# Kernel optimization log

Measured on AMD Instinct MI355X. Metric: run time of the kernel, lower is better.

The kernel has to match this reference:

```python
import jax, jax.numpy as jnp
import numpy as np


def setup_inputs() -> dict:
    key = jax.random.key(0)
    ks = jax.random.split(key, 8)
    B, T, D, S, E, V = 8, 64, 1024, 32, 16, 50257
    SCALE = 0.02  # keep dot-products in a sane range for softmax
    return {
        "decoder_states": jax.random.normal(ks[0], (B, T, D), jnp.float32),
        "scene_memory": jax.random.normal(ks[1], (B, S, D), jnp.float32),
        "embedding_weight": jax.random.normal(ks[2], (V, D), jnp.float32) * SCALE,
        "ent_ids": jax.random.randint(ks[3], (B, S, E), 0, V, jnp.int32),
        "Wq": jax.random.normal(ks[4], (D, D), jnp.float32) * SCALE,
        "bq": jnp.zeros((D,), jnp.float32),
        "Wk": jax.random.normal(ks[5], (D, D), jnp.float32) * SCALE,
        "bk": jnp.zeros((D,), jnp.float32),
        "Wp": jax.random.normal(ks[6], (2 * D, 1), jnp.float32) * SCALE,
        "bp": jnp.full((1,), 3.0, jnp.float32),  # nn.init.constant_(bias, 3.0)
    }


def reference(decoder_states, scene_memory, embedding_weight, ent_ids,
              Wq, bq, Wk, bk, Wp, bp):
    B, T, D = decoder_states.shape
    S = scene_memory.shape[1]
    V = embedding_weight.shape[0]

    # scene-level attention
    q = decoder_states @ Wq + bq            # [B,T,D]
    k = scene_memory @ Wk + bk              # [B,S,D]
    scores = jnp.einsum('btd,bsd->bts', q, k) / jnp.sqrt(jnp.float32(D))
    scene_attn = jax.nn.softmax(scores, axis=-1)          # [B,T,S]
    context = jnp.einsum('bts,bsd->btd', scene_attn, scene_memory)

    # hard p_gen gate
    gate_in = jnp.concatenate([decoder_states, context], axis=-1)  # [B,T,2D]
    p_gen = jax.nn.sigmoid((gate_in @ Wp + bp - 0.5) * 10.0)       # [B,T,1]

    # entity salience per scene, scattered into V-sized tensor
    dec_last = decoder_states[:, -1, :]                   # [B,D]
    ent_embs = embedding_weight[ent_ids]                  # [B,S,E,D] gather
    salience = jax.nn.softmax(
        jnp.einsum('bd,bsed->bse', dec_last, ent_embs), axis=-1)  # [B,S,E]
    bi = jnp.arange(B)[:, None, None]
    si = jnp.arange(S)[None, :, None]
    scene_to_token = jnp.zeros((B, S, V), decoder_states.dtype)
    scene_to_token = scene_to_token.at[bi, si, ent_ids].set(salience)

    pointer_probs = jnp.einsum('bts,bsv->btv', scene_attn, scene_to_token)
    return p_gen, pointer_probs
```

## Files before the change

### kernel.cpp

```cpp
#include <hip/hip_runtime.h>
#include <hip/hip_bf16.h>
#include <math.h>

#define BB 8
#define TT 64
#define DD 1024
#define SS 32
#define EE 16
#define VV 50257
#define BT (BB*TT)
#define BS (BB*SS)

typedef __attribute__((ext_vector_type(8))) short short8;
typedef __attribute__((ext_vector_type(4))) float floatx4;

static __device__ inline unsigned short f2bf(float x) {
    __hip_bfloat16 h = __float2bfloat16(x);
    union { __hip_bfloat16 h; unsigned short u; } cv; cv.h = h;
    return cv.u;
}

static __device__ inline void gl_lds16(const void* g, void* l) {
    __builtin_amdgcn_global_load_lds(
        (const __attribute__((address_space(1))) void*)g,
        (__attribute__((address_space(3))) void*)l, 16, 0, 0);
}

__global__ __launch_bounds__(256) void prep_kernel(
    const float* __restrict__ dec, const float* __restrict__ scene,
    const float* __restrict__ Wq, const float* __restrict__ Wk,
    const float* __restrict__ Wp,
    unsigned short* __restrict__ Xb, unsigned short* __restrict__ Wt,
    float* __restrict__ dw, float* __restrict__ mw)
{
    __shared__ float tile[64][65];
    const int bid = blockIdx.x;
    const int t = threadIdx.x;
    if (bid < 768) {
        const int row = bid;
        const float* src = (row < BT) ? dec + (size_t)row * DD
                                      : scene + (size_t)(row - BT) * DD;
        const float4 v = *(const float4*)&src[t * 4];
        ushort4 u;
        u.x = f2bf(v.x); u.y = f2bf(v.y); u.z = f2bf(v.z); u.w = f2bf(v.w);
        *(ushort4*)&Xb[(size_t)row * DD + t * 4] = u;
    } else if (bid < 1280) {
        const int tb = bid - 768;
        const int sel = tb >> 8;
        const int tt8 = tb & 255;
        const int k0 = (tt8 >> 4) * 64, n0 = (tt8 & 15) * 64;
        const float* Wsrc = sel ? Wk : Wq;
        const int c4 = (t & 15) * 4;
        #pragma unroll
        for (int i = 0; i < 4; ++i) {
            const int r = (t >> 4) + 16 * i;
            const float4 v = *(const float4*)&Wsrc[(size_t)(k0 + r) * DD + n0 + c4];
            tile[r][c4 + 0] = v.x; tile[r][c4 + 1] = v.y;
            tile[r][c4 + 2] = v.z; tile[r][c4 + 3] = v.w;
        }
        __syncthreads();
        #pragma unroll
        for (int i = 0; i < 4; ++i) {
            const int n = (t >> 4) + 16 * i;
            ushort4 u;
            u.x = f2bf(tile[c4 + 0][n]); u.y = f2bf(tile[c4 + 1][n]);
            u.z = f2bf(tile[c4 + 2][n]); u.w = f2bf(tile[c4 + 3][n]);
            *(ushort4*)&Wt[(size_t)sel * DD * DD + (size_t)(n0 + n) * DD + k0 + c4] = u;
        }
    } else {
        const int di = bid - 1280;
        const float* x; const float* wp; float* outp;
        if (di < BT) { x = dec   + (size_t)di * DD;        wp = Wp;      outp = dw + di; }
        else         { x = scene + (size_t)(di - BT) * DD; wp = Wp + DD; outp = mw + (di - BT); }
        float s = 0.f;
        #pragma unroll
        for (int i = 0; i < 4; ++i) s += x[t + 256 * i] * wp[t + 256 * i];
        for (int off = 32; off; off >>= 1) s += __shfl_down(s, off);
        if ((t & 63) == 0) tile[0][t >> 6] = s;
        __syncthreads();
        if (t == 0) *outp = tile[0][0] + tile[0][1] + tile[0][2] + tile[0][3];
    }
}

__global__ __launch_bounds__(128) void gemm_mfma(
    const unsigned short* __restrict__ Xb, const unsigned short* __restrict__ Wt,
    const float* __restrict__ bq, const float* __restrict__ bk,
    float* __restrict__ qo, float* __restrict__ ko)
{
    __shared__ unsigned short As[32 * 32];
    __shared__ unsigned short Bs[64 * 32];
    const int bid = blockIdx.x;
    const int bm = bid >> 4;
    const int bn = bid & 15;
    const int m0 = bm * 32, n0 = bn * 64;
    const bool isq = (bm < 16);
    const unsigned short* Wsel = Wt + (isq ? 0 : (size_t)DD * DD);
    const int tid = threadIdx.x;
    const int w = tid >> 6, l = tid & 63;

    const int arow = 16 * w + (l >> 2);
    const int kb8  = (l & 3) * 8;
    floatx4 acc[4] = {{0.f,0.f,0.f,0.f},{0.f,0.f,0.f,0.f},
                      {0.f,0.f,0.f,0.f},{0.f,0.f,0.f,0.f}};

    for (int k0 = 0; k0 < DD; k0 += 32) {
        __syncthreads();
        gl_lds16(&Xb[(size_t)(m0 + arow) * DD + k0 + kb8], &As[w * 512]);
        #pragma unroll
        for (int i = 0; i < 2; ++i) {
            const int brow = 32 * w + 16 * i + (l >> 2);
            gl_lds16(&Wsel[(size_t)(n0 + brow) * DD + k0 + kb8],
                     &Bs[w * 1024 + i * 512]);
        }
        __syncthreads();
        const short8 a = *(const short8*)&As[(16 * w + (l & 15)) * 32 + (l >> 4) * 8];
        #pragma unroll
        for (int j = 0; j < 4; ++j) {
            const short8 b = *(const short8*)&Bs[(16 * j + (l & 15)) * 32 + (l >> 4) * 8];
            acc[j] = __builtin_amdgcn_mfma_f32_16x16x32_bf16(a, b, acc[j], 0, 0, 0);
        }
    }
    #pragma unroll
    for (int j = 0; j < 4; ++j) {
        const int gcol = n0 + 16 * j + (l & 15);
        const float bias = isq ? bq[gcol] : bk[gcol];
        #pragma unroll
        for (int r = 0; r < 4; ++r) {
            const int grow = m0 + 16 * w + (l >> 4) * 4 + r;
            const float val = acc[j][r] + bias;
            if (isq) qo[(size_t)grow * DD + gcol] = val;
            else     ko[(size_t)(grow - BT) * DD + gcol] = val;
        }
    }
}

__global__ __launch_bounds__(256) void attn_sal_kernel(
    const float* __restrict__ qm, const float* __restrict__ km,
    const float* __restrict__ dec, const float* __restrict__ emb,
    const int* __restrict__ ids,
    const float* __restrict__ dwv, const float* __restrict__ mwv,
    const float* __restrict__ bp,
    float* __restrict__ attn_out, float* __restrict__ pgen_out,
    float* __restrict__ sal_out)
{
    __shared__ __align__(16) float qs[DD];
    __shared__ float sc[SS];
    __shared__ int lid[EE];
    const int tid = threadIdx.x;
    const int w = tid >> 6, lane = tid & 63;

    if (blockIdx.x < BT) {
        const int bt = blockIdx.x;
        const int b  = bt / TT;
        *(float4*)&qs[tid * 4] = *(const float4*)&qm[(size_t)bt * DD + tid * 4];
        __syncthreads();
        for (int j = 0; j < 8; ++j) {
            const int s = w * 8 + j;
            const float* kr = km + (size_t)(b * SS + s) * DD;
            float accv = 0.f;
            #pragma unroll
            for (int i = 0; i < 4; ++i) {
                const float4 qv = *(const float4*)&qs[4 * lane + 256 * i];
                const float4 kv = *(const float4*)&kr[4 * lane + 256 * i];
                accv += qv.x * kv.x + qv.y * kv.y + qv.z * kv.z + qv.w * kv.w;
            }
            for (int off = 32; off; off >>= 1) accv += __shfl_down(accv, off);
            if (lane == 0) sc[s] = accv * 0.03125f;
        }
        __syncthreads();
        if (tid < 64) {
            float v = (lane < SS) ? sc[lane] : -INFINITY;
            float m = v;
            for (int off = 32; off; off >>= 1) m = fmaxf(m, __shfl_xor(m, off));
            float e = (lane < SS) ? __expf(v - m) : 0.f;
            float sum = e;
            for (int off = 32; off; off >>= 1) sum += __shfl_xor(sum, off);
            const float a = e / sum;
            float g = (lane < SS) ? a * mwv[b * SS + lane] : 0.f;
            for (int off = 32; off; off >>= 1) g += __shfl_xor(g, off);
            if (lane < SS) attn_out[bt * SS + lane] = a;
            if (lane == 0) {
                const float z = dwv[bt] + g + bp[0] - 0.5f;
                pgen_out[bt] = 1.0f / (1.0f + __expf(-10.0f * z));
            }
        }
    } else {
        const int bs = blockIdx.x - BT;
        const int b  = bs / SS;
        const float* dl = dec + (size_t)(b * TT + (TT - 1)) * DD;
        *(float4*)&qs[tid * 4] = *(const float4*)&dl[tid * 4];
        if (tid < EE) lid[tid] = ids[bs * EE + tid];
        __syncthreads();
        for (int j = 0; j < 4; ++j) {
            const int e = w * 4 + j;
            const float* er = emb + (size_t)lid[e] * DD;
            float accv = 0.f;
            #pragma unroll
            for (int i = 0; i < 4; ++i) {
                const float4 dv = *(const float4*)&qs[4 * lane + 256 * i];
                const float4 ev = *(const float4*)&er[4 * lane + 256 * i];
                accv += dv.x * ev.x + dv.y * ev.y + dv.z * ev.z + dv.w * ev.w;
            }
            for (int off = 32; off; off >>= 1) accv += __shfl_down(accv, off);
            if (lane == 0) sc[e] = accv;
        }
        __syncthreads();
        if (tid == 0) {
            float m = -INFINITY;
            for (int e = 0; e < EE; ++e) m = fmaxf(m, sc[e]);
            float ex[EE]; float sum = 0.f;
            for (int e = 0; e < EE; ++e) { ex[e] = __expf(sc[e] - m); sum += ex[e]; }
            const float inv = 1.0f / sum;
            for (int e = 0; e < EE; ++e) {
                bool dup = false;
                for (int e2 = e + 1; e2 < EE; ++e2)
                    if (lid[e2] == lid[e]) { dup = true; break; }
                sal_out[bs * EE + e] = dup ? 0.f : ex[e] * inv;
            }
        }
    }
}

__global__ __launch_bounds__(256) void pp_kernel(
    const float* __restrict__ attn, const float* __restrict__ sal,
    const int* __restrict__ ids, float* __restrict__ pp)
{
    __shared__ float at[SS];
    const int bt = blockIdx.x;
    const int b  = bt / TT;
    const int tid = threadIdx.x;
    if (tid < SS) at[tid] = attn[bt * SS + tid];
    float* row = pp + (size_t)bt * VV;
    const int h = (4 - (bt & 3)) & 3;
    if (tid < h) row[tid] = 0.f;
    const int nv = (VV - h) >> 2;
    float4* rv = (float4*)(row + h);
    const float4 z4 = make_float4(0.f, 0.f, 0.f, 0.f);
    for (int i = tid; i < nv; i += 256) rv[i] = z4;
    const int tail = (VV - h) & 3;
    if (tid < tail) row[h + 4 * nv + tid] = 0.f;
    __syncthreads();
    for (int i = tid; i < SS * EE; i += 256) {
        const int s = i >> 4, e = i & 15;
        const float v = at[s] * sal[(b * SS + s) * EE + e];
        atomicAdd(&row[ids[(b * SS + s) * EE + e]], v);
    }
}

extern "C" void kernel_launch(void* const* d_in, const int* in_sizes, int n_in,
                              void* d_out, int out_size, void* d_ws, size_t ws_size,
                              hipStream_t stream) {
    (void)in_sizes; (void)n_in; (void)ws_size; (void)out_size;
    const float* dec   = (const float*)d_in[0];
    const float* scene = (const float*)d_in[1];
    const float* emb   = (const float*)d_in[2];
    const int*   ids   = (const int*)  d_in[3];
    const float* Wq    = (const float*)d_in[4];
    const float* bq    = (const float*)d_in[5];
    const float* Wk    = (const float*)d_in[6];
    const float* bk    = (const float*)d_in[7];
    const float* Wp    = (const float*)d_in[8];
    const float* bp    = (const float*)d_in[9];
    float* out = (float*)d_out;
    float* ws  = (float*)d_ws;

    float* q    = ws;
    float* kbuf = q    + 512 * 1024;
    float* attn = kbuf + 256 * 1024;
    float* sal  = attn + 512 * 32;
    float* dw   = sal  + 256 * 16;
    float* mw   = dw   + 512;
    unsigned short* Xb = (unsigned short*)(mw + 256);
    unsigned short* Wt = Xb + 768 * 1024;

    prep_kernel<<<2048, 256, 0, stream>>>(dec, scene, Wq, Wk, Wp, Xb, Wt, dw, mw);
    gemm_mfma<<<384, 128, 0, stream>>>(Xb, Wt, bq, bk, q, kbuf);
    attn_sal_kernel<<<768, 256, 0, stream>>>(q, kbuf, dec, emb, ids, dw, mw, bp,
                                             attn, out, sal);
    pp_kernel<<<512, 256, 0, stream>>>(attn, sal, ids, out + 512);
}
```

Before: 327.4 us.

## Distribute pointer-prob zeroing across earlier kernels as extra blocks

The roughly 100 MB zero-fill of the pointer_probs output moves out of the final scatter kernel. It is split into three ranges, each handled by extra blocks appended to the prep, GEMM and attention kernels, so the memset overlaps with compute-bound blocks. The scatter kernel then only does the atomic adds. This relies on the float4 view of the output being aligned, since out+512 floats is 16-byte aligned. The extra blocks may compete with the compute blocks for bandwidth and occupancy.

```diff
diff --git a/kernel.cpp b/kernel.cpp
--- a/kernel.cpp
+++ b/kernel.cpp
@@ -11,6 +11,13 @@
 #define BT (BB*TT)
 #define BS (BB*SS)
 
+#define N4TOT 6432896
+#define Z0END 2144300
+#define Z1END 4288600
+#define ZB0 512
+#define ZB1 1024
+#define ZB2 512
+
 typedef __attribute__((ext_vector_type(8))) short short8;
 typedef __attribute__((ext_vector_type(4))) float floatx4;
 
@@ -24,6 +31,13 @@
     __builtin_amdgcn_global_load_lds(
         (const __attribute__((address_space(1))) void*)g,
         (__attribute__((address_space(3))) void*)l, 16, 0, 0);
+}
+
+static __device__ inline void zero_range(float4* pv, int start, int end,
+                                         int zb, int nzb, int nthr) {
+    const float4 z4 = make_float4(0.f, 0.f, 0.f, 0.f);
+    for (int i = start + zb * nthr + (int)threadIdx.x; i < end; i += nzb * nthr)
+        pv[i] = z4;
 }
 
 __global__ __launch_bounds__(256) void prep_kernel(
@@ -31,7 +45,8 @@
     const float* __restrict__ Wq, const float* __restrict__ Wk,
     const float* __restrict__ Wp,
     unsigned short* __restrict__ Xb, unsigned short* __restrict__ Wt,
-    float* __restrict__ dw, float* __restrict__ mw)
+    float* __restrict__ dw, float* __restrict__ mw,
+    float* __restrict__ pp)
 {
     __shared__ float tile[64][65];
     const int bid = blockIdx.x;
@@ -67,7 +82,7 @@
             u.z = f2bf(tile[c4 + 2][n]); u.w = f2bf(tile[c4 + 3][n]);
             *(ushort4*)&Wt[(size_t)sel * DD * DD + (size_t)(n0 + n) * DD + k0 + c4] = u;
         }
-    } else {
+    } else if (bid < 2048) {
         const int di = bid - 1280;
         const float* x; const float* wp; float* outp;
         if (di < BT) { x = dec   + (size_t)di * DD;        wp = Wp;      outp = dw + di; }
@@ -79,17 +94,24 @@
         if ((t & 63) == 0) tile[0][t >> 6] = s;
         __syncthreads();
         if (t == 0) *outp = tile[0][0] + tile[0][1] + tile[0][2] + tile[0][3];
+    } else {
+        zero_range((float4*)pp, 0, Z0END, bid - 2048, ZB0, 256);
     }
 }
 
 __global__ __launch_bounds__(128) void gemm_mfma(
     const unsigned short* __restrict__ Xb, const unsigned short* __restrict__ Wt,
     const float* __restrict__ bq, const float* __restrict__ bk,
-    float* __restrict__ qo, float* __restrict__ ko)
+    float* __restrict__ qo, float* __restrict__ ko,
+    float* __restrict__ pp)
 {
     __shared__ unsigned short As[32 * 32];
     __shared__ unsigned short Bs[64 * 32];
     const int bid = blockIdx.x;
+    if (bid >= 384) {
+        zero_range((float4*)pp, Z0END, Z1END, bid - 384, ZB1, 128);
+        return;
+    }
     const int bm = bid >> 4;
     const int bn = bid & 15;
     const int m0 = bm * 32, n0 = bn * 64;
@@ -141,7 +163,7 @@
     const float* __restrict__ dwv, const float* __restrict__ mwv,
     const float* __restrict__ bp,
     float* __restrict__ attn_out, float* __restrict__ pgen_out,
-    float* __restrict__ sal_out)
+    float* __restrict__ sal_out, float* __restrict__ pp)
 {
     __shared__ __align__(16) float qs[DD];
     __shared__ float sc[SS];
@@ -184,7 +206,7 @@
                 pgen_out[bt] = 1.0f / (1.0f + __expf(-10.0f * z));
             }
         }
-    } else {
+    } else if (blockIdx.x < BT + BS) {
         const int bs = blockIdx.x - BT;
         const int b  = bs / SS;
         const float* dl = dec + (size_t)(b * TT + (TT - 1)) * DD;
@@ -218,10 +240,12 @@
                 sal_out[bs * EE + e] = dup ? 0.f : ex[e] * inv;
             }
         }
-    }
-}
-
-__global__ __launch_bounds__(256) void pp_kernel(
+    } else {
+        zero_range((float4*)pp, Z1END, N4TOT, blockIdx.x - (BT + BS), ZB2, 256);
+    }
+}
+
+__global__ __launch_bounds__(256) void scatter_kernel(
     const float* __restrict__ attn, const float* __restrict__ sal,
     const int* __restrict__ ids, float* __restrict__ pp)
 {
@@ -230,16 +254,8 @@
     const int b  = bt / TT;
     const int tid = threadIdx.x;
     if (tid < SS) at[tid] = attn[bt * SS + tid];
+    __syncthreads();
     float* row = pp + (size_t)bt * VV;
-    const int h = (4 - (bt & 3)) & 3;
-    if (tid < h) row[tid] = 0.f;
-    const int nv = (VV - h) >> 2;
-    float4* rv = (float4*)(row + h);
-    const float4 z4 = make_float4(0.f, 0.f, 0.f, 0.f);
-    for (int i = tid; i < nv; i += 256) rv[i] = z4;
-    const int tail = (VV - h) & 3;
-    if (tid < tail) row[h + 4 * nv + tid] = 0.f;
-    __syncthreads();
     for (int i = tid; i < SS * EE; i += 256) {
         const int s = i >> 4, e = i & 15;
         const float v = at[s] * sal[(b * SS + s) * EE + e];
@@ -263,6 +279,7 @@
     const float* bp    = (const float*)d_in[9];
     float* out = (float*)d_out;
     float* ws  = (float*)d_ws;
+    float* pp  = out + 512;
 
     float* q    = ws;
     float* kbuf = q    + 512 * 1024;
@@ -273,9 +290,10 @@
     unsigned short* Xb = (unsigned short*)(mw + 256);
     unsigned short* Wt = Xb + 768 * 1024;
 
-    prep_kernel<<<2048, 256, 0, stream>>>(dec, scene, Wq, Wk, Wp, Xb, Wt, dw, mw);
-    gemm_mfma<<<384, 128, 0, stream>>>(Xb, Wt, bq, bk, q, kbuf);
-    attn_sal_kernel<<<768, 256, 0, stream>>>(q, kbuf, dec, emb, ids, dw, mw, bp,
-                                             attn, out, sal);
-    pp_kernel<<<512, 256, 0, stream>>>(attn, sal, ids, out + 512);
-}
+    prep_kernel<<<2048 + ZB0, 256, 0, stream>>>(dec, scene, Wq, Wk, Wp,
+                                                Xb, Wt, dw, mw, pp);
+    gemm_mfma<<<384 + ZB1, 128, 0, stream>>>(Xb, Wt, bq, bk, q, kbuf, pp);
+    attn_sal_kernel<<<768 + ZB2, 256, 0, stream>>>(q, kbuf, dec, emb, ids,
+                                                   dw, mw, bp, attn, out, sal, pp);
+    scatter_kernel<<<512, 256, 0, stream>>>(attn, sal, ids, pp);
+}
```

New measurement: 328.2 us. No clear change (+0.3%).

## Fuse attention into pointer scatter, move salience into prep, double-buffer GEMM

Applied to the files above, without the earlier changes.

Salience computation moves from the attention kernel into the prep kernel as extra blocks, since it depends only on the inputs. Scene attention, the softmax and p_gen are fused into the pointer-probability kernel, which removes the attn round trip and one launch. The Q/K GEMM now uses 64x64 tiles with 256 threads and double-buffered LDS staging to prefetch the next K slice while computing. Risks are fewer GEMM blocks (192) lowering occupancy, and longer per-block work in the fused kernel.

```diff
diff --git a/kernel.cpp b/kernel.cpp
--- a/kernel.cpp
+++ b/kernel.cpp
@@ -29,11 +29,13 @@
 __global__ __launch_bounds__(256) void prep_kernel(
     const float* __restrict__ dec, const float* __restrict__ scene,
     const float* __restrict__ Wq, const float* __restrict__ Wk,
-    const float* __restrict__ Wp,
+    const float* __restrict__ Wp, const float* __restrict__ emb,
+    const int* __restrict__ ids,
     unsigned short* __restrict__ Xb, unsigned short* __restrict__ Wt,
-    float* __restrict__ dw, float* __restrict__ mw)
+    float* __restrict__ dw, float* __restrict__ mw,
+    float* __restrict__ sal_out)
 {
-    __shared__ float tile[64][65];
+    __shared__ __align__(16) float tile[64][65];
     const int bid = blockIdx.x;
     const int t = threadIdx.x;
     if (bid < 768) {
@@ -67,7 +69,7 @@
             u.z = f2bf(tile[c4 + 2][n]); u.w = f2bf(tile[c4 + 3][n]);
             *(ushort4*)&Wt[(size_t)sel * DD * DD + (size_t)(n0 + n) * DD + k0 + c4] = u;
         }
-    } else {
+    } else if (bid < 2048) {
         const int di = bid - 1280;
         const float* x; const float* wp; float* outp;
         if (di < BT) { x = dec   + (size_t)di * DD;        wp = Wp;      outp = dw + di; }
@@ -79,137 +81,37 @@
         if ((t & 63) == 0) tile[0][t >> 6] = s;
         __syncthreads();
         if (t == 0) *outp = tile[0][0] + tile[0][1] + tile[0][2] + tile[0][3];
-    }
-}
-
-__global__ __launch_bounds__(128) void gemm_mfma(
-    const unsigned short* __restrict__ Xb, const unsigned short* __restrict__ Wt,
-    const float* __restrict__ bq, const float* __restrict__ bk,
-    float* __restrict__ qo, float* __restrict__ ko)
-{
-    __shared__ unsigned short As[32 * 32];
-    __shared__ unsigned short Bs[64 * 32];
-    const int bid = blockIdx.x;
-    const int bm = bid >> 4;
-    const int bn = bid & 15;
-    const int m0 = bm * 32, n0 = bn * 64;
-    const bool isq = (bm < 16);
-    const unsigned short* Wsel = Wt + (isq ? 0 : (size_t)DD * DD);
-    const int tid = threadIdx.x;
-    const int w = tid >> 6, l = tid & 63;
-
-    const int arow = 16 * w + (l >> 2);
-    const int kb8  = (l & 3) * 8;
-    floatx4 acc[4] = {{0.f,0.f,0.f,0.f},{0.f,0.f,0.f,0.f},
-                      {0.f,0.f,0.f,0.f},{0.f,0.f,0.f,0.f}};
-
-    for (int k0 = 0; k0 < DD; k0 += 32) {
-        __syncthreads();
-        gl_lds16(&Xb[(size_t)(m0 + arow) * DD + k0 + kb8], &As[w * 512]);
-        #pragma unroll
-        for (int i = 0; i < 2; ++i) {
-            const int brow = 32 * w + 16 * i + (l >> 2);
-            gl_lds16(&Wsel[(size_t)(n0 + brow) * DD + k0 + kb8],
-                     &Bs[w * 1024 + i * 512]);
-        }
-        __syncthreads();
-        const short8 a = *(const short8*)&As[(16 * w + (l & 15)) * 32 + (l >> 4) * 8];
-        #pragma unroll
-        for (int j = 0; j < 4; ++j) {
-            const short8 b = *(const short8*)&Bs[(16 * j + (l & 15)) * 32 + (l >> 4) * 8];
-            acc[j] = __builtin_amdgcn_mfma_f32_16x16x32_bf16(a, b, acc[j], 0, 0, 0);
-        }
-    }
-    #pragma unroll
-    for (int j = 0; j < 4; ++j) {
-        const int gcol = n0 + 16 * j + (l & 15);
-        const float bias = isq ? bq[gcol] : bk[gcol];
-        #pragma unroll
-        for (int r = 0; r < 4; ++r) {
-            const int grow = m0 + 16 * w + (l >> 4) * 4 + r;
-            const float val = acc[j][r] + bias;
-            if (isq) qo[(size_t)grow * DD + gcol] = val;
-            else     ko[(size_t)(grow - BT) * DD + gcol] = val;
-        }
-    }
-}
-
-__global__ __launch_bounds__(256) void attn_sal_kernel(
-    const float* __restrict__ qm, const float* __restrict__ km,
-    const float* __restrict__ dec, const float* __restrict__ emb,
-    const int* __restrict__ ids,
-    const float* __restrict__ dwv, const float* __restrict__ mwv,
-    const float* __restrict__ bp,
-    float* __restrict__ attn_out, float* __restrict__ pgen_out,
-    float* __restrict__ sal_out)
-{
-    __shared__ __align__(16) float qs[DD];
-    __shared__ float sc[SS];
-    __shared__ int lid[EE];
-    const int tid = threadIdx.x;
-    const int w = tid >> 6, lane = tid & 63;
-
-    if (blockIdx.x < BT) {
-        const int bt = blockIdx.x;
-        const int b  = bt / TT;
-        *(float4*)&qs[tid * 4] = *(const float4*)&qm[(size_t)bt * DD + tid * 4];
-        __syncthreads();
-        for (int j = 0; j < 8; ++j) {
-            const int s = w * 8 + j;
-            const float* kr = km + (size_t)(b * SS + s) * DD;
-            float accv = 0.f;
-            #pragma unroll
-            for (int i = 0; i < 4; ++i) {
-                const float4 qv = *(const float4*)&qs[4 * lane + 256 * i];
-                const float4 kv = *(const float4*)&kr[4 * lane + 256 * i];
-                accv += qv.x * kv.x + qv.y * kv.y + qv.z * kv.z + qv.w * kv.w;
-            }
-            for (int off = 32; off; off >>= 1) accv += __shfl_down(accv, off);
-            if (lane == 0) sc[s] = accv * 0.03125f;
-        }
-        __syncthreads();
-        if (tid < 64) {
-            float v = (lane < SS) ? sc[lane] : -INFINITY;
-            float m = v;
-            for (int off = 32; off; off >>= 1) m = fmaxf(m, __shfl_xor(m, off));
-            float e = (lane < SS) ? __expf(v - m) : 0.f;
-            float sum = e;
-            for (int off = 32; off; off >>= 1) sum += __shfl_xor(sum, off);
-            const float a = e / sum;
-            float g = (lane < SS) ? a * mwv[b * SS + lane] : 0.f;
-            for (int off = 32; off; off >>= 1) g += __shfl_xor(g, off);
-            if (lane < SS) attn_out[bt * SS + lane] = a;
-            if (lane == 0) {
-                const float z = dwv[bt] + g + bp[0] - 0.5f;
-                pgen_out[bt] = 1.0f / (1.0f + __expf(-10.0f * z));
-            }
-        }
     } else {
-        const int bs = blockIdx.x - BT;
+        __shared__ float logit[EE];
+        __shared__ int lid[EE];
+        const int bs = bid - 2048;
         const int b  = bs / SS;
+        const int w = t >> 6, lane = t & 63;
         const float* dl = dec + (size_t)(b * TT + (TT - 1)) * DD;
-        *(float4*)&qs[tid * 4] = *(const float4*)&dl[tid * 4];
-        if (tid < EE) lid[tid] = ids[bs * EE + tid];
-        __syncthreads();
+        *(float4*)&tile[t >> 4][(t & 15) * 4] = *(const float4*)&dl[t * 4];
+        if (t < EE) lid[t] = ids[bs * EE + t];
+        __syncthreads();
+        const float* dsx = &tile[0][0];
         for (int j = 0; j < 4; ++j) {
             const int e = w * 4 + j;
             const float* er = emb + (size_t)lid[e] * DD;
             float accv = 0.f;
             #pragma unroll
             for (int i = 0; i < 4; ++i) {
-                const float4 dv = *(const float4*)&qs[4 * lane + 256 * i];
-                const float4 ev = *(const float4*)&er[4 * lane + 256 * i];
+                const int idx = 4 * lane + 256 * i;
+                const float4 dv = *(const float4*)&tile[idx >> 6][idx & 63];
+                const float4 ev = *(const float4*)&er[idx];
                 accv += dv.x * ev.x + dv.y * ev.y + dv.z * ev.z + dv.w * ev.w;
             }
             for (int off = 32; off; off >>= 1) accv += __shfl_down(accv, off);
-            if (lane == 0) sc[e] = accv;
-        }
-        __syncthreads();
-        if (tid == 0) {
+            if (lane == 0) logit[e] = accv;
+        }
+        __syncthreads();
+        if (t == 0) {
             float m = -INFINITY;
-            for (int e = 0; e < EE; ++e) m = fmaxf(m, sc[e]);
+            for (int e = 0; e < EE; ++e) m = fmaxf(m, logit[e]);
             float ex[EE]; float sum = 0.f;
-            for (int e = 0; e < EE; ++e) { ex[e] = __expf(sc[e] - m); sum += ex[e]; }
+            for (int e = 0; e < EE; ++e) { ex[e] = __expf(logit[e] - m); sum += ex[e]; }
             const float inv = 1.0f / sum;
             for (int e = 0; e < EE; ++e) {
                 bool dup = false;
@@ -218,18 +120,116 @@
                 sal_out[bs * EE + e] = dup ? 0.f : ex[e] * inv;
             }
         }
-    }
-}
-
-__global__ __launch_bounds__(256) void pp_kernel(
-    const float* __restrict__ attn, const float* __restrict__ sal,
-    const int* __restrict__ ids, float* __restrict__ pp)
+        (void)dsx;
+    }
+}
+
+__global__ __launch_bounds__(256) void gemm_mfma(
+    const unsigned short* __restrict__ Xb, const unsigned short* __restrict__ Wt,
+    const float* __restrict__ bq, const float* __restrict__ bk,
+    float* __restrict__ qo, float* __restrict__ ko)
 {
+    __shared__ unsigned short As[2][64 * 64];
+    __shared__ unsigned short Bs[2][64 * 64];
+    const int bid = blockIdx.x;
+    const int bm = bid >> 4;
+    const int bn = bid & 15;
+    const int m0 = bm * 64, n0 = bn * 64;
+    const bool isq = (bm < 8);
+    const unsigned short* Xrow = Xb + (size_t)m0 * DD;
+    const unsigned short* Wsel = Wt + (isq ? 0 : (size_t)DD * DD) + (size_t)n0 * DD;
+    const int tid = threadIdx.x;
+    const int w = tid >> 6, l = tid & 63;
+
+    const int srow0 = tid >> 3, sko0 = (tid & 7) * 8;
+    const int srow1 = (256 + tid) >> 3, sko1 = sko0;
+    #define STAGE(buf, k0)                                                    \
+        do {                                                                  \
+            gl_lds16(&Xrow[(size_t)srow0 * DD + (k0) + sko0],                 \
+                     &As[buf][(0 * 256 + w * 64) * 8]);                       \
+            gl_lds16(&Wsel[(size_t)srow0 * DD + (k0) + sko0],                 \
+                     &Bs[buf][(0 * 256 + w * 64) * 8]);                       \
+            gl_lds16(&Xrow[(size_t)srow1 * DD + (k0) + sko1],                 \
+                     &As[buf][(1 * 256 + w * 64) * 8]);                       \
+            gl_lds16(&Wsel[(size_t)srow1 * DD + (k0) + sko1],                 \
+                     &Bs[buf][(1 * 256 + w * 64) * 8]);                       \
+        } while (0)
+
+    const int mw_ = (w & 1) * 32;
+    const int nw_ = (w >> 1) * 32;
+    const int fi = l & 15;
+    const int fk = (l >> 4) * 8;
+    floatx4 acc[2][2] = {{{0.f,0.f,0.f,0.f},{0.f,0.f,0.f,0.f}},
+                         {{0.f,0.f,0.f,0.f},{0.f,0.f,0.f,0.f}}};
+
+    STAGE(0, 0);
+    for (int ks = 0; ks < 16; ++ks) {
+        const int cur = ks & 1;
+        __syncthreads();
+        if (ks < 15) STAGE(1 - cur, (ks + 1) * 64);
+        #pragma unroll
+        for (int kk = 0; kk < 2; ++kk) {
+            const short8 a0 = *(const short8*)&As[cur][(mw_ +  0 + fi) * 64 + kk * 32 + fk];
+            const short8 a1 = *(const short8*)&As[cur][(mw_ + 16 + fi) * 64 + kk * 32 + fk];
+            const short8 b0 = *(const short8*)&Bs[cur][(nw_ +  0 + fi) * 64 + kk * 32 + fk];
+            const short8 b1 = *(const short8*)&Bs[cur][(nw_ + 16 + fi) * 64 + kk * 32 + fk];
+            acc[0][0] = __builtin_amdgcn_mfma_f32_16x16x32_bf16(a0, b0, acc[0][0], 0, 0, 0);
+            acc[0][1] = __builtin_amdgcn_mfma_f32_16x16x32_bf16(a0, b1, acc[0][1], 0, 0, 0);
+            acc[1][0] = __builtin_amdgcn_mfma_f32_16x16x32_bf16(a1, b0, acc[1][0], 0, 0, 0);
+            acc[1][1] = __builtin_amdgcn_mfma_f32_16x16x32_bf16(a1, b1, acc[1][1], 0, 0, 0);
+        }
+    }
+    #undef STAGE
+    #pragma unroll
+    for (int mi = 0; mi < 2; ++mi) {
+        #pragma unroll
+        for (int ni = 0; ni < 2; ++ni) {
+            const int gcol = n0 + nw_ + ni * 16 + fi;
+            const float bias = isq ? bq[gcol] : bk[gcol];
+            #pragma unroll
+            for (int r = 0; r < 4; ++r) {
+                const int grow = m0 + mw_ + mi * 16 + (l >> 4) * 4 + r;
+                const float val = acc[mi][ni][r] + bias;
+                if (isq) qo[(size_t)grow * DD + gcol] = val;
+                else     ko[(size_t)(grow - BT) * DD + gcol] = val;
+            }
+        }
+    }
+}
+
+__global__ __launch_bounds__(256) void attn_pp_kernel(
+    const float* __restrict__ qm, const float* __restrict__ km,
+    const float* __restrict__ sal, const int* __restrict__ ids,
+    const float* __restrict__ dwv, const float* __restrict__ mwv,
+    const float* __restrict__ bp,
+    float* __restrict__ pgen_out, float* __restrict__ pp)
+{
+    __shared__ __align__(16) float qs[DD];
+    __shared__ float sc[SS];
     __shared__ float at[SS];
+    __shared__ float salsh[SS * EE];
     const int bt = blockIdx.x;
     const int b  = bt / TT;
     const int tid = threadIdx.x;
-    if (tid < SS) at[tid] = attn[bt * SS + tid];
+    const int w = tid >> 6, lane = tid & 63;
+
+    *(float4*)&qs[tid * 4] = *(const float4*)&qm[(size_t)bt * DD + tid * 4];
+    salsh[tid]       = sal[b * SS * EE + tid];
+    salsh[tid + 256] = sal[b * SS * EE + tid + 256];
+    __syncthreads();
+    for (int j = 0; j < 8; ++j) {
+        const int s = w * 8 + j;
+        const float* kr = km + (size_t)(b * SS + s) * DD;
+        float accv = 0.f;
+        #pragma unroll
+        for (int i = 0; i < 4; ++i) {
+            const float4 qv = *(const float4*)&qs[4 * lane + 256 * i];
+            const float4 kv = *(const float4*)&kr[4 * lane + 256 * i];
+            accv += qv.x * kv.x + qv.y * kv.y + qv.z * kv.z + qv.w * kv.w;
+        }
+        for (int off = 32; off; off >>= 1) accv += __shfl_down(accv, off);
+        if (lane == 0) sc[s] = accv * 0.03125f;
+    }
     float* row = pp + (size_t)bt * VV;
     const int h = (4 - (bt & 3)) & 3;
     if (tid < h) row[tid] = 0.f;
@@ -240,10 +240,29 @@
     const int tail = (VV - h) & 3;
     if (tid < tail) row[h + 4 * nv + tid] = 0.f;
     __syncthreads();
-    for (int i = tid; i < SS * EE; i += 256) {
-        const int s = i >> 4, e = i & 15;
-        const float v = at[s] * sal[(b * SS + s) * EE + e];
-        atomicAdd(&row[ids[(b * SS + s) * EE + e]], v);
+    if (tid < 64) {
+        float v = (lane < SS) ? sc[lane] : -INFINITY;
+        float m = v;
+        for (int off = 32; off; off >>= 1) m = fmaxf(m, __shfl_xor(m, off));
+        float e = (lane < SS) ? __expf(v - m) : 0.f;
+        float sum = e;
+        for (int off = 32; off; off >>= 1) sum += __shfl_xor(sum, off);
+        const float a = e / sum;
+        float g = (lane < SS) ? a * mwv[b * SS + lane] : 0.f;
+        for (int off = 32; off; off >>= 1) g += __shfl_xor(g, off);
+        if (lane < SS) at[lane] = a;
+        if (lane == 0) {
+            const float z = dwv[bt] + g + bp[0] - 0.5f;
+            pgen_out[bt] = 1.0f / (1.0f + __expf(-10.0f * z));
+        }
+    }
+    __syncthreads();
+    const int* idrow = ids + b * SS * EE;
+    #pragma unroll
+    for (int u = 0; u < 2; ++u) {
+        const int i = tid + 256 * u;
+        const float v = at[i >> 4] * salsh[i];
+        atomicAdd(&row[idrow[i]], v);
     }
 }
 
@@ -263,19 +282,19 @@
     const float* bp    = (const float*)d_in[9];
     float* out = (float*)d_out;
     float* ws  = (float*)d_ws;
+    float* pp  = out + 512;
 
     float* q    = ws;
     float* kbuf = q    + 512 * 1024;
-    float* attn = kbuf + 256 * 1024;
-    float* sal  = attn + 512 * 32;
+    float* sal  = kbuf + 256 * 1024;
     float* dw   = sal  + 256 * 16;
     float* mw   = dw   + 512;
     unsigned short* Xb = (unsigned short*)(mw + 256);
     unsigned short* Wt = Xb + 768 * 1024;
 
-    prep_kernel<<<2048, 256, 0, stream>>>(dec, scene, Wq, Wk, Wp, Xb, Wt, dw, mw);
-    gemm_mfma<<<384, 128, 0, stream>>>(Xb, Wt, bq, bk, q, kbuf);
-    attn_sal_kernel<<<768, 256, 0, stream>>>(q, kbuf, dec, emb, ids, dw, mw, bp,
-                                             attn, out, sal);
-    pp_kernel<<<512, 256, 0, stream>>>(attn, sal, ids, out + 512);
-}
+    prep_kernel<<<2304, 256, 0, stream>>>(dec, scene, Wq, Wk, Wp, emb, ids,
+                                          Xb, Wt, dw, mw, sal);
+    gemm_mfma<<<192, 256, 0, stream>>>(Xb, Wt, bq, bk, q, kbuf);
+    attn_pp_kernel<<<512, 256, 0, stream>>>(q, kbuf, sal, ids, dw, mw, bp,
+                                            out, pp);
+}
```

Result: no change. 333.5 us (+1.9%).
